# Kernel optimization log

Measured on AMD Instinct MI355X. Metric: run time of the kernel, lower is better.

Reference implementation:

```python
import jax, jax.numpy as jnp
import numpy as np

B, T, D, H, R, K = 64, 2048, 256, 256, 64, 8
NUM_LEVELS = 5  # height of the 8-ary tree over 2048 nodes (levels 0..4)


def _gru(x, h, w_ih, w_hh, b_ih, b_hh):
    # torch.nn.GRUCell math
    gi = x @ w_ih.T + b_ih          # [N, 3H]
    gh = h @ w_hh.T + b_hh          # [N, 3H]
    i_r, i_z, i_n = jnp.split(gi, 3, axis=-1)
    h_r, h_z, h_n = jnp.split(gh, 3, axis=-1)
    r = jax.nn.sigmoid(i_r + h_r)
    z = jax.nn.sigmoid(i_z + h_z)
    n = jnp.tanh(i_n + r * h_n)
    return (1.0 - z) * n + z * h


def setup_inputs() -> dict:
    key = jax.random.key(0)
    ks = jax.random.split(key, 11)
    s = 1.0 / np.sqrt(H)
    embs = jax.random.normal(ks[0], (B, T, D), jnp.float32)
    rel_emb = (jax.random.normal(ks[1], (R, D), jnp.float32) * s).at[0].set(0.0)  # padding_idx=0
    node_w_ih = jax.random.uniform(ks[2], (3 * H, D), jnp.float32, -s, s)
    node_w_hh = jax.random.uniform(ks[3], (3 * H, H), jnp.float32, -s, s)
    node_b_ih = jax.random.uniform(ks[4], (3 * H,), jnp.float32, -s, s)
    node_b_hh = jax.random.uniform(ks[5], (3 * H,), jnp.float32, -s, s)
    rel_w_ih = jax.random.uniform(ks[6], (3 * H, D), jnp.float32, -s, s)
    rel_w_hh = jax.random.uniform(ks[7], (3 * H, H), jnp.float32, -s, s)
    rel_b_ih = jax.random.uniform(ks[8], (3 * H,), jnp.float32, -s, s)
    rel_b_hh = jax.random.uniform(ks[9], (3 * H,), jnp.float32, -s, s)
    # Deterministic 8-ary tree per batch element: node t>=1 has parent (t-1)//K, root has -1.
    par = np.full(T, -1, np.int64)
    par[1:] = (np.arange(1, T) - 1) // K
    level = np.zeros(T, np.int64)  # topological level = 1 + max level of children (leaves = 0)
    for t in range(T - 1, 0, -1):
        level[par[t]] = max(level[par[t]], level[t] + 1)
    parents = jnp.tile(jnp.asarray(par, jnp.int32)[None, :], (B, 1))
    levels = jnp.tile(jnp.asarray(level, jnp.int32)[None, :], (B, 1))
    rels = jax.random.randint(ks[10], (B, T), 1, R, jnp.int32)
    return dict(embs=embs, rel_emb=rel_emb,
                node_w_ih=node_w_ih, node_w_hh=node_w_hh, node_b_ih=node_b_ih, node_b_hh=node_b_hh,
                rel_w_ih=rel_w_ih, rel_w_hh=rel_w_hh, rel_b_ih=rel_b_ih, rel_b_hh=rel_b_hh,
                parents=parents, rels=rels, levels=levels)


def reference(embs, rel_emb, node_w_ih, node_w_hh, node_b_ih, node_b_hh,
              rel_w_ih, rel_w_hh, rel_b_ih, rel_b_hh, parents, rels, levels):
    b, t, d = embs.shape
    n = b * t
    x = embs.reshape(n, d)                       # node input features
    par = parents.reshape(n).astype(jnp.int32)
    lev = levels.reshape(n, 1)
    # one (potential) edge per node: child -> parent; roots (par == -1) scatter to dummy bin n
    batch_off = (jnp.arange(n, dtype=jnp.int32) // t) * t
    dst = jnp.where(par >= 0, batch_off + par, n)
    rel_x = rel_emb[rels.reshape(n)]             # edge feature = rel embedding of child's relation

    h = jnp.zeros((n, H), embs.dtype)
    # per-level topological propagation (DGL prop_nodes): leaves first, root last
    for L in range(NUM_LEVELS):
        msg = _gru(rel_x, h, rel_w_ih, rel_w_hh, rel_b_ih, rel_b_hh)   # message along each edge
        red = jax.ops.segment_sum(msg, dst, num_segments=n + 1)[:n]    # mailbox sum at parents
        h_new = _gru(x, red, node_w_ih, node_w_hh, node_b_ih, node_b_hh)
        h = jnp.where(lev == L, h_new, h)        # only nodes at this topological level update
    return h.reshape(b, t, H)
```

## Files before the change

### kernel.cpp

```cpp
#include <hip/hip_runtime.h>
#include <hip/hip_bf16.h>
#include <cstdint>
#include <cstddef>

#define B_ 64
#define T_ 2048
#define LDP 40

typedef unsigned short ushort_t;
typedef __attribute__((ext_vector_type(8))) short bf16x8;
typedef __attribute__((ext_vector_type(4))) float f32x4;

__device__ __forceinline__ float sigmoidf_(float x){ return 1.f/(1.f+__expf(-x)); }
__device__ __forceinline__ float tanhf_(float x){
  x = fminf(fmaxf(x,-15.f),15.f);
  float e = __expf(2.f*x);
  return (e-1.f)/(e+1.f);
}

__device__ __forceinline__ unsigned f2b_pair(float lo, float hi){
  unsigned a = __float_as_uint(lo), b = __float_as_uint(hi);
  a += 0x7FFFu + ((a>>16)&1u);
  b += 0x7FFFu + ((b>>16)&1u);
  return (a>>16) | (b & 0xFFFF0000u);
}
__device__ __forceinline__ uint4 pack8(float4 x, float4 y){
  uint4 v;
  v.x = f2b_pair(x.x, x.y);
  v.y = f2b_pair(x.z, x.w);
  v.z = f2b_pair(y.x, y.y);
  v.w = f2b_pair(y.z, y.w);
  return v;
}

__global__ __launch_bounds__(256)
void table_kernel(const float* __restrict__ rel_emb, const float* __restrict__ w_ih,
                  const float* __restrict__ b_ih, float* __restrict__ table)
{
  int idx = blockIdx.x*256 + threadIdx.x;
  int r = idx/768, j = idx - r*768;
  const float* e = rel_emb + (size_t)r*256;
  const float* w = w_ih   + (size_t)j*256;
  float acc = 0.f;
  for(int k=0;k<256;k+=4){
    float4 ev = *(const float4*)(e+k);
    float4 wv = *(const float4*)(w+k);
    acc = fmaf(ev.x,wv.x,acc); acc = fmaf(ev.y,wv.y,acc);
    acc = fmaf(ev.z,wv.z,acc); acc = fmaf(ev.w,wv.w,acc);
  }
  table[idx] = acc + b_ih[j];
}

__global__ __launch_bounds__(256)
void wcvt_kernel(const float* __restrict__ a, const float* __restrict__ b, const float* __restrict__ c,
                 ushort_t* __restrict__ oa, ushort_t* __restrict__ ob, ushort_t* __restrict__ oc)
{
  int i = blockIdx.x*256 + threadIdx.x;
  int seg = i / 24576;
  int off = (i - seg*24576) * 8;
  const float* s; ushort_t* d;
  if(seg==0){ s=a; d=oa; } else if(seg==1){ s=b; d=ob; } else { s=c; d=oc; }
  float4 x = *(const float4*)(s+off), y = *(const float4*)(s+off+4);
  *(uint4*)(d+off) = pack8(x,y);
}


template<bool LEAF>
__global__ __launch_bounds__(256)
void node_mfma(const float* __restrict__ embs, const float* __restrict__ red,
               const ushort_t* __restrict__ wih, const ushort_t* __restrict__ whh,
               const float* __restrict__ b_ih, const float* __restrict__ b_hh,
               float* __restrict__ out, int t_lo, unsigned cnt, unsigned Mtot)
{
  __shared__ ushort_t As[128][LDP];
  __shared__ ushort_t Bs[192][LDP];
  const int tid  = threadIdx.x;
  const unsigned Mbase = blockIdx.x*128u;
  const int nb   = blockIdx.y;
  const int lane = tid & 63, w = tid >> 6;
  const int quad = lane >> 4, cl = lane & 15;

  const int srow = tid >> 2;
  const int g8   = (tid & 3) * 8;
  unsigned r0 = Mbase + srow;      if(r0 > Mtot-1) r0 = Mtot-1;
  unsigned r1 = Mbase + srow + 64; if(r1 > Mtot-1) r1 = Mtot-1;
  unsigned b0v = r0 / cnt, t0v = (unsigned)t_lo + (r0 - b0v*cnt);
  unsigned b1v = r1 / cnt, t1v = (unsigned)t_lo + (r1 - b1v*cnt);
  const float* x0p = embs + ((size_t)b0v*T_ + t0v)*256 + g8;
  const float* x1p = embs + ((size_t)b1v*T_ + t1v)*256 + g8;
  const float* rd0p = red + ((size_t)b0v*256 + t0v)*256 + g8;
  const float* rd1p = red + ((size_t)b1v*256 + t1v)*256 + g8;
  const size_t woff0 = ((size_t)(0*256 + nb*64 + srow))*256 + g8;
  const size_t woff1 = ((size_t)(1*256 + nb*64 + srow))*256 + g8;
  const size_t woff2 = ((size_t)(2*256 + nb*64 + srow))*256 + g8;

  f32x4 acc[2][12];
  f32x4 accN2[2][4];
  const f32x4 zz = {0.f,0.f,0.f,0.f};
  #pragma unroll
  for(int i=0;i<2;i++){
    #pragma unroll
    for(int j=0;j<12;j++) acc[i][j] = zz;
    #pragma unroll
    for(int j=0;j<4;j++) accN2[i][j] = zz;
  }

  const int KSTOT = LEAF ? 256 : 512;
  float4 ax0,ay0,ax1,ay1; uint4 w0,w1,w2;

#define NLOAD(KS) do{ \
    const int kk_ = (KS) & 255; \
    const float* A0_ = (LEAF || (KS) < 256) ? x0p : rd0p; \
    const float* A1_ = (LEAF || (KS) < 256) ? x1p : rd1p; \
    const ushort_t* W_ = (LEAF || (KS) < 256) ? wih : whh; \
    ax0 = *(const float4*)(A0_+kk_); ay0 = *(const float4*)(A0_+kk_+4); \
    ax1 = *(const float4*)(A1_+kk_); ay1 = *(const float4*)(A1_+kk_+4); \
    w0 = *(const uint4*)(W_+woff0+kk_); \
    w1 = *(const uint4*)(W_+woff1+kk_); \
    w2 = *(const uint4*)(W_+woff2+kk_); \
  }while(0)

  NLOAD(0);
  #pragma unroll 1
  for(int ks=0; ks<KSTOT; ks+=32){
    __syncthreads();
    *(uint4*)&As[srow     ][g8] = pack8(ax0, ay0);
    *(uint4*)&As[srow + 64][g8] = pack8(ax1, ay1);
    *(uint4*)&Bs[srow      ][g8] = w0;
    *(uint4*)&Bs[srow +  64][g8] = w1;
    *(uint4*)&Bs[srow + 128][g8] = w2;
    __syncthreads();
    if(ks + 32 < KSTOT) NLOAD(ks + 32);
    const bool p1 = (!LEAF) && (ks >= 256);
    bf16x8 af0 = *(const bf16x8*)&As[w*32      + cl][quad*8];
    bf16x8 af1 = *(const bf16x8*)&As[w*32 + 16 + cl][quad*8];
    #pragma unroll
    for(int j=0;j<12;j++){
      bf16x8 bfj = *(const bf16x8*)&Bs[j*16 + cl][quad*8];
      if(j>=8 && p1){
        accN2[0][j-8] = __builtin_amdgcn_mfma_f32_16x16x32_bf16(af0, bfj, accN2[0][j-8], 0,0,0);
        accN2[1][j-8] = __builtin_amdgcn_mfma_f32_16x16x32_bf16(af1, bfj, accN2[1][j-8], 0,0,0);
      } else {
        acc[0][j] = __builtin_amdgcn_mfma_f32_16x16x32_bf16(af0, bfj, acc[0][j], 0,0,0);
        acc[1][j] = __builtin_amdgcn_mfma_f32_16x16x32_bf16(af1, bfj, acc[1][j], 0,0,0);
      }
    }
  }
#undef NLOAD

  float bir[4],biz[4],bin[4],bhr[4],bhz[4],bhn[4];
  #pragma unroll
  for(int c=0;c<4;c++){
    int col = nb*64 + c*16 + cl;
    bir[c]=b_ih[col]; biz[c]=b_ih[256+col]; bin[c]=b_ih[512+col];
    bhr[c]=b_hh[col]; bhz[c]=b_hh[256+col]; bhn[c]=b_hh[512+col];
  }
  #pragma unroll
  for(int i=0;i<2;i++){
    #pragma unroll
    for(int r=0;r<4;r++){
      unsigned gm = Mbase + (unsigned)(w*32 + i*16 + quad*4 + r);
      if(gm > Mtot-1) gm = Mtot-1;
      unsigned b = gm / cnt, t = (unsigned)t_lo + (gm - b*cnt);
      float* orow = out + ((size_t)b*T_ + t)*256;
      const float* rr = red + ((size_t)b*256 + t)*256;
      #pragma unroll
      for(int c=0;c<4;c++){
        int col = nb*64 + c*16 + cl;
        float gr = acc[i][c][r]   + bir[c] + bhr[c];
        float gz = acc[i][4+c][r] + biz[c] + bhz[c];
        float gni = acc[i][8+c][r] + bin[c];
        float hn  = (LEAF ? 0.f : accN2[i][c][r]) + bhn[c];
        float rg = sigmoidf_(gr);
        float zg = sigmoidf_(gz);
        float ng = tanhf_(gni + rg*hn);
        float rv = LEAF ? 0.f : rr[col];
        orow[col] = (1.f-zg)*ng + zg*rv;
      }
    }
  }
}

__global__ __launch_bounds__(256)
void msg_mfma(const float* __restrict__ hbuf, const ushort_t* __restrict__ wbf,
              const float* __restrict__ b_hh, const float* __restrict__ table,
              const int* __restrict__ rels, float* __restrict__ red,
              int t_lo, unsigned cnt, unsigned Mtot)
{
  __shared__ ushort_t As[128][LDP];
  __shared__ ushort_t Bs[192][LDP];
  const int tid  = threadIdx.x;
  const unsigned Mbase = blockIdx.x*128u;
  const int nb   = blockIdx.y;
  const int lane = tid & 63, w = tid >> 6;
  const int quad = lane >> 4, cl = lane & 15;

  const int srow = tid >> 2;
  const int g8   = (tid & 3) * 8;
  unsigned r0 = Mbase + srow;      if(r0 > Mtot-1) r0 = Mtot-1;
  unsigned r1 = Mbase + srow + 64; if(r1 > Mtot-1) r1 = Mtot-1;
  unsigned b0v = r0 / cnt, t0v = (unsigned)t_lo + (r0 - b0v*cnt);
  unsigned b1v = r1 / cnt, t1v = (unsigned)t_lo + (r1 - b1v*cnt);
  const float* a0 = hbuf + ((size_t)b0v*T_ + t0v)*256 + g8;
  const float* a1 = hbuf + ((size_t)b1v*T_ + t1v)*256 + g8;
  const size_t woff0 = ((size_t)(0*256 + nb*64 + srow))*256 + g8;
  const size_t woff1 = ((size_t)(1*256 + nb*64 + srow))*256 + g8;
  const size_t woff2 = ((size_t)(2*256 + nb*64 + srow))*256 + g8;

  f32x4 acc[2][12];
  const f32x4 zz = {0.f,0.f,0.f,0.f};
  #pragma unroll
  for(int i=0;i<2;i++)
    #pragma unroll
    for(int j=0;j<12;j++) acc[i][j] = zz;

  float4 ax0,ay0,ax1,ay1; uint4 w0,w1,w2;

#define MLOAD(KK) do{ \
    ax0 = *(const float4*)(a0+(KK)); ay0 = *(const float4*)(a0+(KK)+4); \
    ax1 = *(const float4*)(a1+(KK)); ay1 = *(const float4*)(a1+(KK)+4); \
    w0 = *(const uint4*)(wbf+woff0+(KK)); \
    w1 = *(const uint4*)(wbf+woff1+(KK)); \
    w2 = *(const uint4*)(wbf+woff2+(KK)); \
  }while(0)

  MLOAD(0);
  #pragma unroll 1
  for(int kk=0; kk<256; kk+=32){
    __syncthreads();
    *(uint4*)&As[srow     ][g8] = pack8(ax0, ay0);
    *(uint4*)&As[srow + 64][g8] = pack8(ax1, ay1);
    *(uint4*)&Bs[srow      ][g8] = w0;
    *(uint4*)&Bs[srow +  64][g8] = w1;
    *(uint4*)&Bs[srow + 128][g8] = w2;
    __syncthreads();
    if(kk + 32 < 256) MLOAD(kk + 32);
    bf16x8 af0 = *(const bf16x8*)&As[w*32      + cl][quad*8];
    bf16x8 af1 = *(const bf16x8*)&As[w*32 + 16 + cl][quad*8];
    #pragma unroll
    for(int j=0;j<12;j++){
      bf16x8 bfj = *(const bf16x8*)&Bs[j*16 + cl][quad*8];
      acc[0][j] = __builtin_amdgcn_mfma_f32_16x16x32_bf16(af0, bfj, acc[0][j], 0,0,0);
      acc[1][j] = __builtin_amdgcn_mfma_f32_16x16x32_bf16(af1, bfj, acc[1][j], 0,0,0);
    }
  }
#undef MLOAD

  float bhr[4],bhz[4],bhn[4];
  #pragma unroll
  for(int c=0;c<4;c++){
    int col = nb*64 + c*16 + cl;
    bhr[c]=b_hh[col]; bhz[c]=b_hh[256+col]; bhn[c]=b_hh[512+col];
  }
  #pragma unroll
  for(int i=0;i<2;i++){
    float* rp[4]; bool okr[4]; const float* tb[4]; const float* hrp[4];
    #pragma unroll
    for(int r=0;r<4;r++){
      unsigned gm = Mbase + (unsigned)(w*32 + i*16 + quad*4 + r);
      okr[r] = (gm < Mtot);
      if(gm > Mtot-1) gm = Mtot-1;
      unsigned b = gm / cnt, t = (unsigned)t_lo + (gm - b*cnt);
      int rel = rels[(size_t)b*T_ + t];
      tb[r]  = table + (size_t)rel*768;
      hrp[r] = hbuf + ((size_t)b*T_ + t)*256;
      rp[r]  = red + ((size_t)b*256 + ((t-1)>>3))*256;
    }
    float mv[4][4];
    #pragma unroll
    for(int r=0;r<4;r++){
      #pragma unroll
      for(int c=0;c<4;c++){
        int col = nb*64 + c*16 + cl;
        float gr  = tb[r][col]     + acc[i][c][r]   + bhr[c];
        float gz  = tb[r][256+col] + acc[i][4+c][r] + bhz[c];
        float gnh = acc[i][8+c][r] + bhn[c];
        float rg = sigmoidf_(gr);
        float zg = sigmoidf_(gz);
        float ng = tanhf_(tb[r][512+col] + rg*gnh);
        mv[r][c] = (1.f-zg)*ng + zg*hrp[r][col];
      }
    }
    #pragma unroll
    for(int c=0;c<4;c++){
      int col = nb*64 + c*16 + cl;
      float a = 0.f; bool any = false;
      #pragma unroll
      for(int r=0;r<4;r++){
        if(okr[r]){ a += mv[r][c]; any = true; }
        bool flush;
        if(r==3) flush = true; else flush = (rp[r+1] != rp[r]);
        if(flush){
          if(any) atomicAdd(rp[r] + col, a);
          a = 0.f; any = false;
        }
      }
    }
  }
}

extern "C" void kernel_launch(void* const* d_in, const int* in_sizes, int n_in,
                              void* d_out, int out_size, void* d_ws, size_t ws_size,
                              hipStream_t stream)
{
  const float* embs    = (const float*)d_in[0];
  const float* rel_emb = (const float*)d_in[1];
  const float* nwih    = (const float*)d_in[2];
  const float* nwhh    = (const float*)d_in[3];
  const float* nbih    = (const float*)d_in[4];
  const float* nbhh    = (const float*)d_in[5];
  const float* rwih    = (const float*)d_in[6];
  const float* rwhh    = (const float*)d_in[7];
  const float* rbih    = (const float*)d_in[8];
  const float* rbhh    = (const float*)d_in[9];
  const int*   rels    = (const int*)d_in[11];
  float* out = (float*)d_out;

  float* red   = (float*)d_ws;
  float* table = red + (size_t)4194304;
  ushort_t* wih_bf  = (ushort_t*)(table + 49152);
  ushort_t* whh_bf  = wih_bf + 196608;
  ushort_t* rwhh_bf = whh_bf + 196608;

  hipMemsetAsync(red, 0, (size_t)4194304*4, stream);
  table_kernel<<<dim3(192), 256, 0, stream>>>(rel_emb, rwih, rbih, table);
  wcvt_kernel<<<dim3(288), 256, 0, stream>>>(nwih, nwhh, rwhh, wih_bf, whh_bf, rwhh_bf);

  const int      tlo[5] = {256, 32, 4, 1, 0};
  const unsigned cntv[5]= {1792, 224, 28, 3, 1};
  const unsigned Mv[5]  = {114688, 14336, 1792, 192, 64};

  for(int L=0; L<5; L++){
    dim3 g((Mv[L]+127)/128, 4);
    if(L==0)
      node_mfma<true ><<<g, 256, 0, stream>>>(embs, red, wih_bf, whh_bf, nbih, nbhh, out, tlo[L], cntv[L], Mv[L]);
    else
      node_mfma<false><<<g, 256, 0, stream>>>(embs, red, wih_bf, whh_bf, nbih, nbhh, out, tlo[L], cntv[L], Mv[L]);
    if(L < 4)
      msg_mfma<<<g, 256, 0, stream>>>(out, rwhh_bf, rbhh, table, rels, red, tlo[L], cntv[L], Mv[L]);
  }
}
```

Before: 717.4 us.

## Fuse leaf-level node GRU and message GRU into one kernel

Adds a leaf_fused kernel that, for each 128-row tile of leaf nodes, computes the node GRU (x@Wih) across all 768 output columns and then the message GRU (h@rwhh) with atomic scatter into the parent mailboxes. The embeddings are packed to bf16 once into a full-K LDS tile, and weight tiles are double-buffered. This replaces the two separate level-0 launches, which each used a 4-way column-block grid and re-read the input rows. It trades launch count and repeated A loads for fewer blocks (896 instead of 3584) and a long serial loop per block, which may reduce parallelism and occupancy.

```diff
diff --git a/kernel.cpp b/kernel.cpp
--- a/kernel.cpp
+++ b/kernel.cpp
@@ -6,6 +6,8 @@
 #define B_ 64
 #define T_ 2048
 #define LDP 40
+#define AXP 264
+#define BSP 36
 
 typedef unsigned short ushort_t;
 typedef __attribute__((ext_vector_type(8))) short bf16x8;
@@ -62,6 +64,192 @@
   if(seg==0){ s=a; d=oa; } else if(seg==1){ s=b; d=ob; } else { s=c; d=oc; }
   float4 x = *(const float4*)(s+off), y = *(const float4*)(s+off+4);
   *(uint4*)(d+off) = pack8(x,y);
+}
+
+__global__ __launch_bounds__(256)
+void leaf_fused(const float* __restrict__ embs,
+                const ushort_t* __restrict__ wih,
+                const ushort_t* __restrict__ rwhh,
+                const float* __restrict__ nbih, const float* __restrict__ nbhh,
+                const float* __restrict__ rbhh,
+                const float* __restrict__ table, const int* __restrict__ rels,
+                float* __restrict__ out, float* __restrict__ red)
+{
+  __shared__ ushort_t Ax[128][AXP];
+  __shared__ ushort_t Bs[2][192][BSP];
+
+  const int tid  = threadIdx.x;
+  const unsigned Mbase = blockIdx.x*128u;
+  const int lane = tid & 63, w = tid >> 6;
+  const int quad = lane >> 4, cl = lane & 15;
+  const int srow = tid >> 2;
+  const int g8   = (tid & 3) * 8;
+
+  unsigned r0 = Mbase + srow, r1 = r0 + 64;
+  unsigned b0 = r0 / 1792u, t0 = 256u + (r0 - b0*1792u);
+  unsigned b1 = r1 / 1792u, t1 = 256u + (r1 - b1*1792u);
+  const float* x0p = embs + ((size_t)b0*T_ + t0)*256 + g8;
+  const float* x1p = embs + ((size_t)b1*T_ + t1)*256 + g8;
+  const float* o0p = out  + ((size_t)b0*T_ + t0)*256 + g8;
+  const float* o1p = out  + ((size_t)b1*T_ + t1)*256 + g8;
+
+  const size_t wb0 = ((size_t)(0*256 + srow))*256 + g8;
+  const size_t wb1 = ((size_t)(1*256 + srow))*256 + g8;
+  const size_t wb2 = ((size_t)(2*256 + srow))*256 + g8;
+
+  f32x4 acc[2][12];
+  const f32x4 zz = {0.f,0.f,0.f,0.f};
+  #pragma unroll
+  for(int i=0;i<2;i++)
+    #pragma unroll
+    for(int j=0;j<12;j++) acc[i][j] = zz;
+
+  float4 ax0,ay0,ax1,ay1; uint4 wq0,wq1,wq2;
+
+#define LOADB(S) do{ const ushort_t* Wm_ = ((S) < 32) ? wih : rwhh; \
+    const size_t off_ = (size_t)(((((S)>>3)&3)*16384) + (((S)&7)*32)); \
+    wq0 = *(const uint4*)(Wm_ + wb0 + off_); \
+    wq1 = *(const uint4*)(Wm_ + wb1 + off_); \
+    wq2 = *(const uint4*)(Wm_ + wb2 + off_); }while(0)
+#define LOADA(S) do{ const int kk_ = (S)*32; \
+    ax0 = *(const float4*)(x0p+kk_); ay0 = *(const float4*)(x0p+kk_+4); \
+    ax1 = *(const float4*)(x1p+kk_); ay1 = *(const float4*)(x1p+kk_+4); }while(0)
+
+  LOADA(0); LOADB(0);
+  *(uint4*)&Ax[srow    ][g8] = pack8(ax0,ay0);
+  *(uint4*)&Ax[srow+64 ][g8] = pack8(ax1,ay1);
+  *(uint4*)&Bs[0][srow     ][g8] = wq0;
+  *(uint4*)&Bs[0][srow+64  ][g8] = wq1;
+  *(uint4*)&Bs[0][srow+128 ][g8] = wq2;
+  LOADA(1); LOADB(1);
+  __syncthreads();
+
+  #pragma unroll 1
+  for(int s=0; s<64; ++s){
+    if(s == 32){
+      #pragma unroll
+      for(int kk2=0; kk2<256; kk2+=32){
+        float4 h0 = *(const float4*)(o0p + kk2);
+        float4 h1 = *(const float4*)(o0p + kk2 + 4);
+        float4 h2 = *(const float4*)(o1p + kk2);
+        float4 h3 = *(const float4*)(o1p + kk2 + 4);
+        *(uint4*)&Ax[srow   ][kk2 + g8] = pack8(h0,h1);
+        *(uint4*)&Ax[srow+64][kk2 + g8] = pack8(h2,h3);
+      }
+      __syncthreads();
+    }
+    const int k = s & 7;
+    const int p = s & 1;
+    bf16x8 af0 = *(const bf16x8*)&Ax[w*32      + cl][k*32 + quad*8];
+    bf16x8 af1 = *(const bf16x8*)&Ax[w*32 + 16 + cl][k*32 + quad*8];
+    #pragma unroll
+    for(int j=0;j<12;j++){
+      bf16x8 bfj = *(const bf16x8*)&Bs[p][j*16+cl][quad*8];
+      acc[0][j] = __builtin_amdgcn_mfma_f32_16x16x32_bf16(af0, bfj, acc[0][j], 0,0,0);
+      acc[1][j] = __builtin_amdgcn_mfma_f32_16x16x32_bf16(af1, bfj, acc[1][j], 0,0,0);
+    }
+    if(s < 63){
+      *(uint4*)&Bs[p^1][srow     ][g8] = wq0;
+      *(uint4*)&Bs[p^1][srow+64  ][g8] = wq1;
+      *(uint4*)&Bs[p^1][srow+128 ][g8] = wq2;
+    }
+    if(s+1 < 8){
+      *(uint4*)&Ax[srow    ][(s+1)*32 + g8] = pack8(ax0,ay0);
+      *(uint4*)&Ax[srow+64 ][(s+1)*32 + g8] = pack8(ax1,ay1);
+    }
+    if(s+2 <= 63) LOADB(s+2);
+    if(s+2 <  8) LOADA(s+2);
+
+    if(k == 7){
+      const int e = s >> 3;
+      if(e < 4){
+        const int nb = e;
+        float bir[4],biz[4],bin[4],bhr[4],bhz[4],bhn[4];
+        #pragma unroll
+        for(int c=0;c<4;c++){
+          int col = nb*64 + c*16 + cl;
+          bir[c]=nbih[col]; biz[c]=nbih[256+col]; bin[c]=nbih[512+col];
+          bhr[c]=nbhh[col]; bhz[c]=nbhh[256+col]; bhn[c]=nbhh[512+col];
+        }
+        #pragma unroll
+        for(int i=0;i<2;i++){
+          #pragma unroll
+          for(int r=0;r<4;r++){
+            const int lr = w*32 + i*16 + quad*4 + r;
+            unsigned gm = Mbase + (unsigned)lr;
+            unsigned b = gm / 1792u, t = 256u + (gm - b*1792u);
+            float* orow = out + ((size_t)b*T_ + t)*256;
+            #pragma unroll
+            for(int c=0;c<4;c++){
+              int col = nb*64 + c*16 + cl;
+              float gr  = acc[i][c][r]   + bir[c] + bhr[c];
+              float gz  = acc[i][4+c][r] + biz[c] + bhz[c];
+              float gni = acc[i][8+c][r] + bin[c];
+              float rg = sigmoidf_(gr);
+              float zg = sigmoidf_(gz);
+              float ng = tanhf_(gni + rg*bhn[c]);
+              orow[col] = (1.f - zg)*ng;
+            }
+          }
+        }
+      } else {
+        const int nb = e - 4;
+        float mhr[4],mhz[4],mhn[4];
+        #pragma unroll
+        for(int c=0;c<4;c++){
+          int col = nb*64 + c*16 + cl;
+          mhr[c]=rbhh[col]; mhz[c]=rbhh[256+col]; mhn[c]=rbhh[512+col];
+        }
+        #pragma unroll
+        for(int i=0;i<2;i++){
+          const float* tbp[4]; const float* hp[4]; float* rp[4];
+          #pragma unroll
+          for(int r=0;r<4;r++){
+            const int lr = w*32 + i*16 + quad*4 + r;
+            unsigned gm = Mbase + (unsigned)lr;
+            unsigned b = gm / 1792u, t = 256u + (gm - b*1792u);
+            int rel = rels[(size_t)b*T_ + t];
+            tbp[r] = table + (size_t)rel*768;
+            hp[r]  = out + ((size_t)b*T_ + t)*256;
+            rp[r]  = red + ((size_t)b*256 + ((t-1)>>3))*256;
+          }
+          float mv[4][4];
+          #pragma unroll
+          for(int r=0;r<4;r++){
+            #pragma unroll
+            for(int c=0;c<4;c++){
+              int col = nb*64 + c*16 + cl;
+              float gr  = tbp[r][col]     + acc[i][c][r]   + mhr[c];
+              float gz  = tbp[r][256+col] + acc[i][4+c][r] + mhz[c];
+              float gnh = acc[i][8+c][r] + mhn[c];
+              float rg = sigmoidf_(gr);
+              float zg = sigmoidf_(gz);
+              float ng = tanhf_(tbp[r][512+col] + rg*gnh);
+              mv[r][c] = (1.f-zg)*ng + zg*hp[r][col];
+            }
+          }
+          #pragma unroll
+          for(int c=0;c<4;c++){
+            int col = nb*64 + c*16 + cl;
+            float a = mv[0][c];
+            #pragma unroll
+            for(int r=1;r<4;r++){
+              if(rp[r] != rp[r-1]){ atomicAdd(rp[r-1] + col, a); a = 0.f; }
+              a += mv[r][c];
+            }
+            atomicAdd(rp[3] + col, a);
+          }
+        }
+      }
+      #pragma unroll
+      for(int i=0;i<2;i++)
+        #pragma unroll
+        for(int j=0;j<12;j++) acc[i][j] = zz;
+    }
+    __syncthreads();
+  }
+#undef LOADB
+#undef LOADA
 }
 
 
@@ -326,16 +514,16 @@
   table_kernel<<<dim3(192), 256, 0, stream>>>(rel_emb, rwih, rbih, table);
   wcvt_kernel<<<dim3(288), 256, 0, stream>>>(nwih, nwhh, rwhh, wih_bf, whh_bf, rwhh_bf);
 
+  leaf_fused<<<dim3(896), 256, 0, stream>>>(embs, wih_bf, rwhh_bf,
+                                            nbih, nbhh, rbhh, table, rels, out, red);
+
   const int      tlo[5] = {256, 32, 4, 1, 0};
   const unsigned cntv[5]= {1792, 224, 28, 3, 1};
   const unsigned Mv[5]  = {114688, 14336, 1792, 192, 64};
 
-  for(int L=0; L<5; L++){
+  for(int L=1; L<5; L++){
     dim3 g((Mv[L]+127)/128, 4);
-    if(L==0)
-      node_mfma<true ><<<g, 256, 0, stream>>>(embs, red, wih_bf, whh_bf, nbih, nbhh, out, tlo[L], cntv[L], Mv[L]);
-    else
-      node_mfma<false><<<g, 256, 0, stream>>>(embs, red, wih_bf, whh_bf, nbih, nbhh, out, tlo[L], cntv[L], Mv[L]);
+    node_mfma<false><<<g, 256, 0, stream>>>(embs, red, wih_bf, whh_bf, nbih, nbhh, out, tlo[L], cntv[L], Mv[L]);
     if(L < 4)
       msg_mfma<<<g, 256, 0, stream>>>(out, rwhh_bf, rbhh, table, rels, red, tlo[L], cntv[L], Mv[L]);
   }
```

New measurement: 828.6 us. +15.5%, slower.

## Stream weight tiles directly into double-buffered LDS and prefetch activations two stages ahead

Applied to the files above, without the earlier changes.

In both the node and message GEMM kernels, weight tiles are now copied from global memory straight into LDS with global_load_lds, into two ping-pong buffers. The activation tile is still converted to bf16 through registers, but is prefetched two K-steps ahead. The message kernel also loads relation indices before the main loop. The aim is to cut register pressure and the VGPR-to-LDS store traffic for weights, and to overlap weight fetches with MFMA work. In exchange the B tile loses its row padding, which can cause LDS bank conflicts, and the code relies on barriers to wait for the asynchronous LDS writes.

```diff
diff --git a/kernel.cpp b/kernel.cpp
--- a/kernel.cpp
+++ b/kernel.cpp
@@ -31,6 +31,12 @@
   v.z = f2b_pair(y.x, y.y);
   v.w = f2b_pair(y.z, y.w);
   return v;
+}
+
+__device__ __forceinline__ void gload_lds16(const ushort_t* g, ushort_t* l){
+  __builtin_amdgcn_global_load_lds(
+      (const __attribute__((address_space(1))) unsigned int*)g,
+      (__attribute__((address_space(3))) unsigned int*)l, 16, 0, 0);
 }
 
 __global__ __launch_bounds__(256)
@@ -73,7 +79,7 @@
                float* __restrict__ out, int t_lo, unsigned cnt, unsigned Mtot)
 {
   __shared__ ushort_t As[128][LDP];
-  __shared__ ushort_t Bs[192][LDP];
+  __shared__ ushort_t Bs[2][192][32];
   const int tid  = threadIdx.x;
   const unsigned Mbase = blockIdx.x*128u;
   const int nb   = blockIdx.y;
@@ -90,9 +96,6 @@
   const float* x1p = embs + ((size_t)b1v*T_ + t1v)*256 + g8;
   const float* rd0p = red + ((size_t)b0v*256 + t0v)*256 + g8;
   const float* rd1p = red + ((size_t)b1v*256 + t1v)*256 + g8;
-  const size_t woff0 = ((size_t)(0*256 + nb*64 + srow))*256 + g8;
-  const size_t woff1 = ((size_t)(1*256 + nb*64 + srow))*256 + g8;
-  const size_t woff2 = ((size_t)(2*256 + nb*64 + srow))*256 + g8;
 
   f32x4 acc[2][12];
   f32x4 accN2[2][4];
@@ -106,47 +109,68 @@
   }
 
   const int KSTOT = LEAF ? 256 : 512;
-  float4 ax0,ay0,ax1,ay1; uint4 w0,w1,w2;
-
-#define NLOAD(KS) do{ \
+  float4 aR[2][4];
+
+#define ALOAD(SET, KS) do{ \
     const int kk_ = (KS) & 255; \
     const float* A0_ = (LEAF || (KS) < 256) ? x0p : rd0p; \
     const float* A1_ = (LEAF || (KS) < 256) ? x1p : rd1p; \
+    aR[SET][0] = *(const float4*)(A0_+kk_); aR[SET][1] = *(const float4*)(A0_+kk_+4); \
+    aR[SET][2] = *(const float4*)(A1_+kk_); aR[SET][3] = *(const float4*)(A1_+kk_+4); \
+  }while(0)
+
+#define BDMA(KS, PN) do{ \
     const ushort_t* W_ = (LEAF || (KS) < 256) ? wih : whh; \
-    ax0 = *(const float4*)(A0_+kk_); ay0 = *(const float4*)(A0_+kk_+4); \
-    ax1 = *(const float4*)(A1_+kk_); ay1 = *(const float4*)(A1_+kk_+4); \
-    w0 = *(const uint4*)(W_+woff0+kk_); \
-    w1 = *(const uint4*)(W_+woff1+kk_); \
-    w2 = *(const uint4*)(W_+woff2+kk_); \
-  }while(0)
-
-  NLOAD(0);
+    const int kk_ = (KS) & 255; \
+    const int ch0_ = w*3; \
+    gload_lds16(W_ + (size_t)((ch0_>>2)*256 + nb*64 + (ch0_&3)*16 + (lane>>2))*256 + kk_ + (lane&3)*8, &Bs[PN][ch0_*16][0]); \
+    const int ch1_ = w*3+1; \
+    gload_lds16(W_ + (size_t)((ch1_>>2)*256 + nb*64 + (ch1_&3)*16 + (lane>>2))*256 + kk_ + (lane&3)*8, &Bs[PN][ch1_*16][0]); \
+    const int ch2_ = w*3+2; \
+    gload_lds16(W_ + (size_t)((ch2_>>2)*256 + nb*64 + (ch2_&3)*16 + (lane>>2))*256 + kk_ + (lane&3)*8, &Bs[PN][ch2_*16][0]); \
+  }while(0)
+
+#define COMPUTE(KS, P) do{ \
+    const bool p1_ = (!LEAF) && ((KS) >= 256); \
+    bf16x8 af0 = *(const bf16x8*)&As[w*32      + cl][quad*8]; \
+    bf16x8 af1 = *(const bf16x8*)&As[w*32 + 16 + cl][quad*8]; \
+    _Pragma("unroll") \
+    for(int j=0;j<12;j++){ \
+      bf16x8 bfj = *(const bf16x8*)&Bs[P][j*16 + cl][quad*8]; \
+      if(j>=8 && p1_){ \
+        accN2[0][j-8] = __builtin_amdgcn_mfma_f32_16x16x32_bf16(af0, bfj, accN2[0][j-8], 0,0,0); \
+        accN2[1][j-8] = __builtin_amdgcn_mfma_f32_16x16x32_bf16(af1, bfj, accN2[1][j-8], 0,0,0); \
+      } else { \
+        acc[0][j] = __builtin_amdgcn_mfma_f32_16x16x32_bf16(af0, bfj, acc[0][j], 0,0,0); \
+        acc[1][j] = __builtin_amdgcn_mfma_f32_16x16x32_bf16(af1, bfj, acc[1][j], 0,0,0); \
+      } \
+    } \
+  }while(0)
+
+  BDMA(0, 0);
+  ALOAD(0, 0);
+  ALOAD(1, 32);
+
   #pragma unroll 1
-  for(int ks=0; ks<KSTOT; ks+=32){
-    __syncthreads();
-    *(uint4*)&As[srow     ][g8] = pack8(ax0, ay0);
-    *(uint4*)&As[srow + 64][g8] = pack8(ax1, ay1);
-    *(uint4*)&Bs[srow      ][g8] = w0;
-    *(uint4*)&Bs[srow +  64][g8] = w1;
-    *(uint4*)&Bs[srow + 128][g8] = w2;
-    __syncthreads();
-    if(ks + 32 < KSTOT) NLOAD(ks + 32);
-    const bool p1 = (!LEAF) && (ks >= 256);
-    bf16x8 af0 = *(const bf16x8*)&As[w*32      + cl][quad*8];
-    bf16x8 af1 = *(const bf16x8*)&As[w*32 + 16 + cl][quad*8];
-    #pragma unroll
-    for(int j=0;j<12;j++){
-      bf16x8 bfj = *(const bf16x8*)&Bs[j*16 + cl][quad*8];
-      if(j>=8 && p1){
-        accN2[0][j-8] = __builtin_amdgcn_mfma_f32_16x16x32_bf16(af0, bfj, accN2[0][j-8], 0,0,0);
-        accN2[1][j-8] = __builtin_amdgcn_mfma_f32_16x16x32_bf16(af1, bfj, accN2[1][j-8], 0,0,0);
-      } else {
-        acc[0][j] = __builtin_amdgcn_mfma_f32_16x16x32_bf16(af0, bfj, acc[0][j], 0,0,0);
-        acc[1][j] = __builtin_amdgcn_mfma_f32_16x16x32_bf16(af1, bfj, acc[1][j], 0,0,0);
-      }
-    }
-  }
-#undef NLOAD
+  for(int kk=0; kk<KSTOT; kk+=64){
+    __syncthreads();
+    *(uint4*)&As[srow   ][g8] = pack8(aR[0][0], aR[0][1]);
+    *(uint4*)&As[srow+64][g8] = pack8(aR[0][2], aR[0][3]);
+    __syncthreads();
+    BDMA(kk+32, 1);
+    if(kk+64 < KSTOT) ALOAD(0, kk+64);
+    COMPUTE(kk, 0);
+    __syncthreads();
+    *(uint4*)&As[srow   ][g8] = pack8(aR[1][0], aR[1][1]);
+    *(uint4*)&As[srow+64][g8] = pack8(aR[1][2], aR[1][3]);
+    __syncthreads();
+    if(kk+64 < KSTOT) BDMA(kk+64, 0);
+    if(kk+96 < KSTOT) ALOAD(1, kk+96);
+    COMPUTE(kk+32, 1);
+  }
+#undef ALOAD
+#undef BDMA
+#undef COMPUTE
 
   float bir[4],biz[4],bin[4],bhr[4],bhz[4],bhn[4];
   #pragma unroll
@@ -188,7 +212,7 @@
               int t_lo, unsigned cnt, unsigned Mtot)
 {
   __shared__ ushort_t As[128][LDP];
-  __shared__ ushort_t Bs[192][LDP];
+  __shared__ ushort_t Bs[2][192][32];
   const int tid  = threadIdx.x;
   const unsigned Mbase = blockIdx.x*128u;
   const int nb   = blockIdx.y;
@@ -203,9 +227,6 @@
   unsigned b1v = r1 / cnt, t1v = (unsigned)t_lo + (r1 - b1v*cnt);
   const float* a0 = hbuf + ((size_t)b0v*T_ + t0v)*256 + g8;
   const float* a1 = hbuf + ((size_t)b1v*T_ + t1v)*256 + g8;
-  const size_t woff0 = ((size_t)(0*256 + nb*64 + srow))*256 + g8;
-  const size_t woff1 = ((size_t)(1*256 + nb*64 + srow))*256 + g8;
-  const size_t woff2 = ((size_t)(2*256 + nb*64 + srow))*256 + g8;
 
   f32x4 acc[2][12];
   const f32x4 zz = {0.f,0.f,0.f,0.f};
@@ -214,37 +235,68 @@
     #pragma unroll
     for(int j=0;j<12;j++) acc[i][j] = zz;
 
-  float4 ax0,ay0,ax1,ay1; uint4 w0,w1,w2;
-
-#define MLOAD(KK) do{ \
-    ax0 = *(const float4*)(a0+(KK)); ay0 = *(const float4*)(a0+(KK)+4); \
-    ax1 = *(const float4*)(a1+(KK)); ay1 = *(const float4*)(a1+(KK)+4); \
-    w0 = *(const uint4*)(wbf+woff0+(KK)); \
-    w1 = *(const uint4*)(wbf+woff1+(KK)); \
-    w2 = *(const uint4*)(wbf+woff2+(KK)); \
-  }while(0)
-
-  MLOAD(0);
+  int relv[2][4];
+  #pragma unroll
+  for(int i=0;i<2;i++)
+    #pragma unroll
+    for(int r=0;r<4;r++){
+      unsigned gm = Mbase + (unsigned)(w*32 + i*16 + quad*4 + r);
+      if(gm > Mtot-1) gm = Mtot-1;
+      unsigned b = gm / cnt, t = (unsigned)t_lo + (gm - b*cnt);
+      relv[i][r] = rels[(size_t)b*T_ + t];
+    }
+
+  float4 aR[2][4];
+
+#define MALOAD(SET, KK) do{ \
+    aR[SET][0] = *(const float4*)(a0+(KK)); aR[SET][1] = *(const float4*)(a0+(KK)+4); \
+    aR[SET][2] = *(const float4*)(a1+(KK)); aR[SET][3] = *(const float4*)(a1+(KK)+4); \
+  }while(0)
+
+#define MBDMA(KK, PN) do{ \
+    const int ch0_ = w*3; \
+    gload_lds16(wbf + (size_t)((ch0_>>2)*256 + nb*64 + (ch0_&3)*16 + (lane>>2))*256 + (KK) + (lane&3)*8, &Bs[PN][ch0_*16][0]); \
+    const int ch1_ = w*3+1; \
+    gload_lds16(wbf + (size_t)((ch1_>>2)*256 + nb*64 + (ch1_&3)*16 + (lane>>2))*256 + (KK) + (lane&3)*8, &Bs[PN][ch1_*16][0]); \
+    const int ch2_ = w*3+2; \
+    gload_lds16(wbf + (size_t)((ch2_>>2)*256 + nb*64 + (ch2_&3)*16 + (lane>>2))*256 + (KK) + (lane&3)*8, &Bs[PN][ch2_*16][0]); \
+  }while(0)
+
+#define MCOMPUTE(P) do{ \
+    bf16x8 af0 = *(const bf16x8*)&As[w*32      + cl][quad*8]; \
+    bf16x8 af1 = *(const bf16x8*)&As[w*32 + 16 + cl][quad*8]; \
+    _Pragma("unroll") \
+    for(int j=0;j<12;j++){ \
+      bf16x8 bfj = *(const bf16x8*)&Bs[P][j*16 + cl][quad*8]; \
+      acc[0][j] = __builtin_amdgcn_mfma_f32_16x16x32_bf16(af0, bfj, acc[0][j], 0,0,0); \
+      acc[1][j] = __builtin_amdgcn_mfma_f32_16x16x32_bf16(af1, bfj, acc[1][j], 0,0,0); \
+    } \
+  }while(0)
+
+  MBDMA(0, 0);
+  MALOAD(0, 0);
+  MALOAD(1, 32);
+
   #pragma unroll 1
-  for(int kk=0; kk<256; kk+=32){
-    __syncthreads();
-    *(uint4*)&As[srow     ][g8] = pack8(ax0, ay0);
-    *(uint4*)&As[srow + 64][g8] = pack8(ax1, ay1);
-    *(uint4*)&Bs[srow      ][g8] = w0;
-    *(uint4*)&Bs[srow +  64][g8] = w1;
-    *(uint4*)&Bs[srow + 128][g8] = w2;
-    __syncthreads();
-    if(kk + 32 < 256) MLOAD(kk + 32);
-    bf16x8 af0 = *(const bf16x8*)&As[w*32      + cl][quad*8];
-    bf16x8 af1 = *(const bf16x8*)&As[w*32 + 16 + cl][quad*8];
-    #pragma unroll
-    for(int j=0;j<12;j++){
-      bf16x8 bfj = *(const bf16x8*)&Bs[j*16 + cl][quad*8];
-      acc[0][j] = __builtin_amdgcn_mfma_f32_16x16x32_bf16(af0, bfj, acc[0][j], 0,0,0);
-      acc[1][j] = __builtin_amdgcn_mfma_f32_16x16x32_bf16(af1, bfj, acc[1][j], 0,0,0);
-    }
-  }
-#undef MLOAD
+  for(int kk=0; kk<256; kk+=64){
+    __syncthreads();
+    *(uint4*)&As[srow   ][g8] = pack8(aR[0][0], aR[0][1]);
+    *(uint4*)&As[srow+64][g8] = pack8(aR[0][2], aR[0][3]);
+    __syncthreads();
+    MBDMA(kk+32, 1);
+    if(kk+64 < 256) MALOAD(0, kk+64);
+    MCOMPUTE(0);
+    __syncthreads();
+    *(uint4*)&As[srow   ][g8] = pack8(aR[1][0], aR[1][1]);
+    *(uint4*)&As[srow+64][g8] = pack8(aR[1][2], aR[1][3]);
+    __syncthreads();
+    if(kk+64 < 256) MBDMA(kk+64, 0);
+    if(kk+96 < 256) MALOAD(1, kk+96);
+    MCOMPUTE(1);
+  }
+#undef MALOAD
+#undef MBDMA
+#undef MCOMPUTE
 
   float bhr[4],bhz[4],bhn[4];
   #pragma unroll
@@ -261,8 +313,7 @@
       okr[r] = (gm < Mtot);
       if(gm > Mtot-1) gm = Mtot-1;
       unsigned b = gm / cnt, t = (unsigned)t_lo + (gm - b*cnt);
-      int rel = rels[(size_t)b*T_ + t];
-      tb[r]  = table + (size_t)rel*768;
+      tb[r]  = table + (size_t)relv[i][r]*768;
       hrp[r] = hbuf + ((size_t)b*T_ + t)*256;
       rp[r]  = red + ((size_t)b*256 + ((t-1)>>3))*256;
     }
```

Measured after the change: 835.7 us. 16.5% more time.
